# Kernel optimization log

Measured on AMD Instinct MI355X. Metric: run time of the kernel, lower is better.

Reference implementation:

```python
import jax, jax.numpy as jnp
import numpy as np

D_MODEL = 64  # angle_dist_dim
IN_CH = 256
EPS = 1e-6


def sinusoidal_embedding(e, d_model):
    # e: (N, K) -> (N, K, d_model), interleaved [sin0, cos0, sin1, cos1, ...]
    div_term = jnp.exp(jnp.arange(0, d_model, 2, dtype=jnp.float32) * (-np.log(10000.0) / d_model))
    om = e[..., None] * div_term  # (N, K, d_model//2)
    emb = jnp.stack([jnp.sin(om), jnp.cos(om)], axis=-1)  # (N, K, d/2, 2)
    return emb.reshape(e.shape + (d_model,))


def setup_inputs() -> dict:
    key = jax.random.key(0)
    ks = jax.random.split(key, 5)
    N, K, C = 40000, 16, IN_CH
    triplet_dim = 2 * C + D_MODEL  # 576
    x = jax.random.normal(ks[0], (N, C), dtype=jnp.float32)
    pos = jax.random.normal(ks[1], (N, 3), dtype=jnp.float32) * 10.0
    anchor_indices = jnp.arange(N, dtype=jnp.int32)
    corner_indices = jax.random.randint(ks[2], (N, K, 2), 0, N, dtype=jnp.int32)
    corner_masks = jnp.ones((N, K), dtype=bool)
    Wqkv_w = jax.random.normal(ks[3], (3 * C, triplet_dim), dtype=jnp.float32) / np.sqrt(triplet_dim)
    Wqkv_b = jax.random.normal(ks[4], (3 * C,), dtype=jnp.float32) * 0.01
    return {"x": x, "pos": pos, "anchor_indices": anchor_indices,
            "corner_indices": corner_indices, "corner_masks": corner_masks,
            "Wqkv_w": Wqkv_w, "Wqkv_b": Wqkv_b}


def reference(x, pos, anchor_indices, corner_indices, corner_masks, Wqkv_w, Wqkv_b):
    N, C = x.shape
    padded_x = jnp.concatenate([x, jnp.zeros((1, C), x.dtype)], axis=0)
    padded_pos = jnp.concatenate([pos, jnp.zeros((1, 3), pos.dtype)], axis=0)

    anchor_p = padded_pos[anchor_indices]            # (Na, 3)
    v0 = padded_pos[corner_indices[:, :, 0]] - anchor_p[:, None]  # (Na, K, 3)
    v1 = padded_pos[corner_indices[:, :, 1]] - anchor_p[:, None]
    v0 = jax.lax.stop_gradient(v0).at[:, :, 2].set(0.0)  # zero z (detached geometry)
    v1 = jax.lax.stop_gradient(v1).at[:, :, 2].set(0.0)

    cos_values = jnp.sum(v0 * v1, axis=-1) / (
        jnp.linalg.norm(v0, axis=-1) * jnp.linalg.norm(v1, axis=-1) + EPS)
    # z-component of cross product (x,y only since z was zeroed)
    sin_z = v0[..., 0] * v1[..., 1] - v0[..., 1] * v1[..., 0]
    reorder = sin_z < 0  # (Na, K)

    ci = jnp.where(reorder[..., None], corner_indices[:, :, ::-1], corner_indices)

    nv0 = jax.lax.stop_gradient(padded_pos[ci[:, :, 0]] - anchor_p[:, None]).at[:, :, 2].set(0.0)
    nv1 = jax.lax.stop_gradient(padded_pos[ci[:, :, 1]] - anchor_p[:, None]).at[:, :, 2].set(0.0)
    new_sin_z = nv0[..., 0] * nv1[..., 1] - nv0[..., 1] * nv1[..., 0]
    # corner_masks is all-True so boolean selection == full flatten (static shape)
    triplet_false_masks = ((new_sin_z < -1e-6) & corner_masks).reshape(-1)

    angle_features = jax.lax.stop_gradient(sinusoidal_embedding(cos_values, D_MODEL))
    triplet_feats = jnp.concatenate(
        [padded_x[ci[:, :, 0]], padded_x[ci[:, :, 1]], angle_features], axis=-1)  # (Na, K, 576)

    qkv = triplet_feats @ Wqkv_w.T + Wqkv_b            # (Na, K, 3C)
    qkv = qkv.reshape(qkv.shape[0], qkv.shape[1], 3, C)
    q, k, v = qkv[:, :, 0], qkv[:, :, 1], qkv[:, :, 2]

    scores = jnp.einsum('nqc,nkc->nqk', q, k) / np.sqrt(C)
    attn = jax.nn.softmax(scores, axis=-1)
    attn_feats = jnp.einsum('nqk,nkc->nqc', attn, v)   # (Na, K, C)

    mask_f = corner_masks.astype(attn_feats.dtype)
    denom = jnp.sum(mask_f, axis=1, keepdims=True)     # (Na, 1)
    mean_feats = jnp.sum(attn_feats * mask_f[..., None], axis=1) / denom  # (Na, C)

    x_messages = jnp.zeros_like(x).at[anchor_indices].set(mean_feats)
    out = jnp.concatenate([x, x_messages], axis=1)     # (N, 2C), triplet_mlp_method='concat'
    return out, triplet_false_masks
```

## Files before the change

### kernel.cpp

```cpp
#include <hip/hip_runtime.h>

typedef unsigned short u16;
typedef __attribute__((ext_vector_type(8))) short short8v;
typedef __attribute__((ext_vector_type(4))) float float4v;

__device__ __forceinline__ float bf2f(u16 u) {
  union { unsigned int i; float f; } v; v.i = ((unsigned int)u) << 16; return v.f;
}
__device__ __forceinline__ u16 f2bf(float f) {
  union { unsigned int i; float f; } v; v.f = f;
  unsigned int r = v.i + 0x7fffu + ((v.i >> 16) & 1u);
  return (u16)(r >> 16);
}
__device__ __forceinline__ float4v mfma_bf16(short8v a, short8v b, float4v c) {
  return __builtin_amdgcn_mfma_f32_16x16x32_bf16(a, b, c, 0, 0, 0);
}

__global__ __launch_bounds__(256) void prep_kernel(const float* __restrict__ W,
                                                   u16* __restrict__ Bt,
                                                   u16* __restrict__ W2t) {
  int j = blockIdx.x;
  int c = threadIdx.x;
  const float* wr = W + (size_t)j * 576;
  Bt[(size_t)j * 256 + c]         = f2bf(wr[c]);
  Bt[(size_t)(768 + j) * 256 + c] = f2bf(wr[256 + c]);
  if (c < 64) W2t[(size_t)j * 64 + c] = f2bf(wr[512 + c]);
}

__global__ __launch_bounds__(256) void gemm_kernel(const float* __restrict__ A,
                                                   const u16* __restrict__ Bt,
                                                   u16* __restrict__ Y, int M) {
  __shared__ __align__(16) u16 As[128][72];
  __shared__ __align__(16) u16 Bs[128][72];
  int tid = threadIdx.x;
  int row0 = blockIdx.x * 128, col0 = blockIdx.y * 128;
  int w = tid >> 6, l = tid & 63;
  int wr = w >> 1, wc = w & 1;
  int lr = l & 15, lq = l >> 4;

  float4v acc[4][4];
#pragma unroll
  for (int mi = 0; mi < 4; mi++)
#pragma unroll
    for (int ni = 0; ni < 4; ni++) acc[mi][ni] = (float4v)0.f;

  for (int k0 = 0; k0 < 256; k0 += 64) {
#pragma unroll
    for (int i = 0; i < 4; i++) {
      int chunk = tid + i * 256;
      int r = chunk >> 3;
      int kc = (chunk & 7) * 8;
      int gr = row0 + r;
      short8v av = (short8v)0;
      if (gr < M) {
        float4 f0 = *(const float4*)(A + (size_t)gr * 256 + k0 + kc);
        float4 f1 = *(const float4*)(A + (size_t)gr * 256 + k0 + kc + 4);
        av[0] = (short)f2bf(f0.x); av[1] = (short)f2bf(f0.y);
        av[2] = (short)f2bf(f0.z); av[3] = (short)f2bf(f0.w);
        av[4] = (short)f2bf(f1.x); av[5] = (short)f2bf(f1.y);
        av[6] = (short)f2bf(f1.z); av[7] = (short)f2bf(f1.w);
      }
      *(short8v*)&As[r][kc] = av;
      short8v bv = *(const short8v*)(Bt + (size_t)(col0 + r) * 256 + k0 + kc);
      *(short8v*)&Bs[r][kc] = bv;
    }
    __syncthreads();
#pragma unroll
    for (int s = 0; s < 2; s++) {
      int kb = s * 32 + lq * 8;
      short8v af[4], bf[4];
#pragma unroll
      for (int mi = 0; mi < 4; mi++)
        af[mi] = *(const short8v*)&As[wr * 64 + mi * 16 + lr][kb];
#pragma unroll
      for (int ni = 0; ni < 4; ni++)
        bf[ni] = *(const short8v*)&Bs[wc * 64 + ni * 16 + lr][kb];
#pragma unroll
      for (int mi = 0; mi < 4; mi++)
#pragma unroll
        for (int ni = 0; ni < 4; ni++)
          acc[mi][ni] = mfma_bf16(af[mi], bf[ni], acc[mi][ni]);
    }
    __syncthreads();
  }
#pragma unroll
  for (int mi = 0; mi < 4; mi++)
#pragma unroll
    for (int ni = 0; ni < 4; ni++) {
      int rbase = row0 + wr * 64 + mi * 16 + lq * 4;
      int c = col0 + wc * 64 + ni * 16 + lr;
#pragma unroll
      for (int j = 0; j < 4; j++) {
        int r = rbase + j;
        if (r < M) Y[(size_t)r * 1536 + c] = f2bf(acc[mi][ni][j]);
      }
    }
}

__global__ __launch_bounds__(256) void triplet_kernel(
    const float* __restrict__ x, const float* __restrict__ pos,
    const int* __restrict__ anchor, const int* __restrict__ corner,
    const float* __restrict__ bias, const u16* __restrict__ Y,
    const u16* __restrict__ W2t, float* __restrict__ out, int N) {
  __shared__ float s_cos[16];
  __shared__ float s_div[32];
  __shared__ int s_i0[16], s_i1[16];
  __shared__ __align__(16) u16 s_qkv[16][776];

  int n = blockIdx.x;
  if (n >= N) return;
  int tid = threadIdx.x;
  int w = tid >> 6;
  int l = tid & 63;
  int lr = l & 15, lq = l >> 4, kg = lq * 8;
  int a = anchor[n];

  if (tid < 32) s_div[tid] = __expf(-0.28782313662425572f * (float)tid);
  if (tid < 16) {
    int t = tid;
    int2 ci = ((const int2*)corner)[n * 16 + t];
    float ax = pos[(size_t)a * 3], ay = pos[(size_t)a * 3 + 1];
    float v0x = pos[(size_t)ci.x * 3]     - ax;
    float v0y = pos[(size_t)ci.x * 3 + 1] - ay;
    float v1x = pos[(size_t)ci.y * 3]     - ax;
    float v1y = pos[(size_t)ci.y * 3 + 1] - ay;
    float dot = v0x * v1x + v0y * v1y;
    float n0 = sqrtf(v0x * v0x + v0y * v0y);
    float n1 = sqrtf(v1x * v1x + v1y * v1y);
    s_cos[t] = dot / (n0 * n1 + 1e-6f);
    float sinz = v0x * v1y - v0y * v1x;
    bool sw = sinz < 0.f;
    s_i0[t] = sw ? ci.y : ci.x;
    s_i1[t] = sw ? ci.x : ci.y;
    __builtin_nontemporal_store(0.0f, &out[(size_t)N * 512 + (size_t)n * 16 + t]);
  }
  if (tid < 64) {
    const float4v* src = (const float4v*)(x + (size_t)n * 256);
    float4v* dst = (float4v*)(out + (size_t)n * 512);
    float4v v = __builtin_nontemporal_load(src + tid);
    __builtin_nontemporal_store(v, dst + tid);
  }
  __syncthreads();

  float cosv = s_cos[lr];
  short8v a0, a1;
#pragma unroll
  for (int jj = 0; jj < 4; jj++) {
    int kh = (kg >> 1) + jj;
    float om0 = cosv * s_div[kh];
    a0[2 * jj]     = (short)f2bf(__sinf(om0));
    a0[2 * jj + 1] = (short)f2bf(__cosf(om0));
    float om1 = cosv * s_div[16 + kh];
    a1[2 * jj]     = (short)f2bf(__sinf(om1));
    a1[2 * jj + 1] = (short)f2bf(__cosf(om1));
  }
  int i0r[4], i1r[4];
#pragma unroll
  for (int j = 0; j < 4; j++) {
    int t = lq * 4 + j;
    i0r[j] = s_i0[t];
    i1r[j] = s_i1[t];
  }

  for (int u = 0; u < 12; u++) {
    int nt = w * 12 + u;
    int col = nt * 16 + lr;
    short8v b0 = *(const short8v*)(W2t + (size_t)col * 64 + kg);
    short8v b1 = *(const short8v*)(W2t + (size_t)col * 64 + 32 + kg);
    float4v acc = (float4v)0.f;
    acc = mfma_bf16(a0, b0, acc);
    acc = mfma_bf16(a1, b1, acc);
    float bs = bias[col];
#pragma unroll
    for (int j = 0; j < 4; j++) {
      float v = acc[j] + bs + bf2f(Y[(size_t)i0r[j] * 1536 + col]) +
                bf2f(Y[(size_t)i1r[j] * 1536 + 768 + col]);
      s_qkv[lq * 4 + j][col] = f2bf(v);
    }
  }
  __syncthreads();

  float4v sa = (float4v)0.f;
#pragma unroll
  for (int cs = 0; cs < 8; cs++) {
    short8v qf = *(const short8v*)&s_qkv[lr][cs * 32 + kg];
    short8v kf = *(const short8v*)&s_qkv[lr][256 + cs * 32 + kg];
    sa = mfma_bf16(qf, kf, sa);
  }
  float wsum = 0.f;
#pragma unroll
  for (int j = 0; j < 4; j++) {
    float s = sa[j] * 0.0625f;
    float m = s;
    m = fmaxf(m, __shfl_xor(m, 1));
    m = fmaxf(m, __shfl_xor(m, 2));
    m = fmaxf(m, __shfl_xor(m, 4));
    m = fmaxf(m, __shfl_xor(m, 8));
    float e = __expf(s - m);
    float sm = e;
    sm += __shfl_xor(sm, 1);
    sm += __shfl_xor(sm, 2);
    sm += __shfl_xor(sm, 4);
    sm += __shfl_xor(sm, 8);
    wsum += e / sm;
  }
  wsum += __shfl_xor(wsum, 16);
  wsum += __shfl_xor(wsum, 32);
  wsum *= 0.0625f;

  int c = (w << 6) + l;
  float o = 0.f;
#pragma unroll
  for (int kk = 0; kk < 16; kk++) {
    float wk = __shfl(wsum, kk);
    o += wk * bf2f(s_qkv[kk][512 + c]);
  }
  __builtin_nontemporal_store(o, &out[(size_t)a * 512 + 256 + c]);
}

extern "C" void kernel_launch(void* const* d_in, const int* in_sizes, int n_in,
                              void* d_out, int out_size, void* d_ws, size_t ws_size,
                              hipStream_t stream) {
  const float* x    = (const float*)d_in[0];
  const float* pos  = (const float*)d_in[1];
  const int* anchor = (const int*)d_in[2];
  const int* corner = (const int*)d_in[3];
  const float* W    = (const float*)d_in[5];
  const float* bias = (const float*)d_in[6];
  float* out = (float*)d_out;
  int N = in_sizes[2];

  char* wsb = (char*)d_ws;
  u16* Bt  = (u16*)wsb;
  u16* W2t = (u16*)(wsb + 786432);
  u16* Y   = (u16*)(wsb + 786432 + 98304);

  prep_kernel<<<768, 256, 0, stream>>>(W, Bt, W2t);
  gemm_kernel<<<dim3((N + 127) / 128, 12), 256, 0, stream>>>(x, Bt, Y, N);
  triplet_kernel<<<N, 256, 0, stream>>>(x, pos, anchor, corner, bias, Y, W2t, out, N);
}
```

Measured before the change: 804.8 us.

## Reassociate V projection after attention averaging to shrink precomputed Y

Before, the kernel precomputed V for every node and gathered it per triplet. Now the attention-weighted mean is applied to the raw gathered x rows and the angle embeddings first, using linearity. The resulting 512-wide per-anchor features S are multiplied by the V weights in a second GEMM that adds bias and accumulates into the output. This drops a third of the first GEMM output and the V gathers, but adds fp32 x gathers in the triplet kernel, a new GEMM pass over N, and a read-modify-write of the output.

```diff
diff --git a/kernel.cpp b/kernel.cpp
--- a/kernel.cpp
+++ b/kernel.cpp
@@ -18,13 +18,21 @@
 
 __global__ __launch_bounds__(256) void prep_kernel(const float* __restrict__ W,
                                                    u16* __restrict__ Bt,
-                                                   u16* __restrict__ W2t) {
+                                                   u16* __restrict__ W2qk,
+                                                   u16* __restrict__ Wvt,
+                                                   u16* __restrict__ Wvat) {
   int j = blockIdx.x;
   int c = threadIdx.x;
   const float* wr = W + (size_t)j * 576;
   Bt[(size_t)j * 256 + c]         = f2bf(wr[c]);
-  Bt[(size_t)(768 + j) * 256 + c] = f2bf(wr[256 + c]);
-  if (c < 64) W2t[(size_t)j * 64 + c] = f2bf(wr[512 + c]);
+  Bt[(size_t)(512 + j) * 256 + c] = f2bf(wr[256 + c]);
+  if (c < 64) W2qk[(size_t)j * 64 + c] = f2bf(wr[512 + c]);
+  if (j < 256) {
+    const float* wv = W + (size_t)(512 + j) * 576;
+    Wvt[(size_t)j * 512 + c]       = f2bf(wv[c]);
+    Wvt[(size_t)j * 512 + 256 + c] = f2bf(wv[256 + c]);
+    if (c < 64) Wvat[(size_t)j * 64 + c] = f2bf(wv[512 + c]);
+  }
 }
 
 __global__ __launch_bounds__(256) void gemm_kernel(const float* __restrict__ A,
@@ -92,7 +100,7 @@
 #pragma unroll
       for (int j = 0; j < 4; j++) {
         int r = rbase + j;
-        if (r < M) Y[(size_t)r * 1536 + c] = f2bf(acc[mi][ni][j]);
+        if (r < M) Y[(size_t)r * 1024 + c] = f2bf(acc[mi][ni][j]);
       }
     }
 }
@@ -100,12 +108,14 @@
 __global__ __launch_bounds__(256) void triplet_kernel(
     const float* __restrict__ x, const float* __restrict__ pos,
     const int* __restrict__ anchor, const int* __restrict__ corner,
-    const float* __restrict__ bias, const u16* __restrict__ Y,
-    const u16* __restrict__ W2t, float* __restrict__ out, int N) {
+    const float* __restrict__ bias, const u16* __restrict__ Yqk,
+    const u16* __restrict__ W2qk, const u16* __restrict__ Wvat,
+    u16* __restrict__ S, float* __restrict__ out, int N) {
   __shared__ float s_cos[16];
   __shared__ float s_div[32];
+  __shared__ float s_sang[64];
   __shared__ int s_i0[16], s_i1[16];
-  __shared__ __align__(16) u16 s_qkv[16][776];
+  __shared__ __align__(16) u16 s_qk[16][520];
 
   int n = blockIdx.x;
   if (n >= N) return;
@@ -162,20 +172,20 @@
     i1r[j] = s_i1[t];
   }
 
-  for (int u = 0; u < 12; u++) {
-    int nt = w * 12 + u;
+  for (int u = 0; u < 8; u++) {
+    int nt = w * 8 + u;
     int col = nt * 16 + lr;
-    short8v b0 = *(const short8v*)(W2t + (size_t)col * 64 + kg);
-    short8v b1 = *(const short8v*)(W2t + (size_t)col * 64 + 32 + kg);
+    short8v b0 = *(const short8v*)(W2qk + (size_t)col * 64 + kg);
+    short8v b1 = *(const short8v*)(W2qk + (size_t)col * 64 + 32 + kg);
     float4v acc = (float4v)0.f;
     acc = mfma_bf16(a0, b0, acc);
     acc = mfma_bf16(a1, b1, acc);
     float bs = bias[col];
 #pragma unroll
     for (int j = 0; j < 4; j++) {
-      float v = acc[j] + bs + bf2f(Y[(size_t)i0r[j] * 1536 + col]) +
-                bf2f(Y[(size_t)i1r[j] * 1536 + 768 + col]);
-      s_qkv[lq * 4 + j][col] = f2bf(v);
+      float v = acc[j] + bs + bf2f(Yqk[(size_t)i0r[j] * 1024 + col]) +
+                bf2f(Yqk[(size_t)i1r[j] * 1024 + 512 + col]);
+      s_qk[lq * 4 + j][col] = f2bf(v);
     }
   }
   __syncthreads();
@@ -183,8 +193,8 @@
   float4v sa = (float4v)0.f;
 #pragma unroll
   for (int cs = 0; cs < 8; cs++) {
-    short8v qf = *(const short8v*)&s_qkv[lr][cs * 32 + kg];
-    short8v kf = *(const short8v*)&s_qkv[lr][256 + cs * 32 + kg];
+    short8v qf = *(const short8v*)&s_qk[lr][cs * 32 + kg];
+    short8v kf = *(const short8v*)&s_qk[lr][256 + cs * 32 + kg];
     sa = mfma_bf16(qf, kf, sa);
   }
   float wsum = 0.f;
@@ -208,14 +218,114 @@
   wsum += __shfl_xor(wsum, 32);
   wsum *= 0.0625f;
 
-  int c = (w << 6) + l;
-  float o = 0.f;
-#pragma unroll
-  for (int kk = 0; kk < 16; kk++) {
-    float wk = __shfl(wsum, kk);
-    o += wk * bf2f(s_qkv[kk][512 + c]);
-  }
-  __builtin_nontemporal_store(o, &out[(size_t)a * 512 + 256 + c]);
+  {
+    int c = tid;
+    float acc0 = 0.f, acc1 = 0.f;
+#pragma unroll
+    for (int t = 0; t < 16; t++) {
+      float wt = __shfl(wsum, t);
+      int r0 = s_i0[t], r1 = s_i1[t];
+      acc0 += wt * x[(size_t)r0 * 256 + c];
+      acc1 += wt * x[(size_t)r1 * 256 + c];
+    }
+    S[(size_t)n * 512 + c]       = f2bf(acc0);
+    S[(size_t)n * 512 + 256 + c] = f2bf(acc1);
+  }
+
+  if (tid < 64) {
+    float dv = s_div[tid >> 1];
+    float sj = 0.f;
+#pragma unroll
+    for (int t = 0; t < 16; t++) {
+      float wt = __shfl(wsum, t);
+      float om = s_cos[t] * dv;
+      sj += wt * ((tid & 1) ? __cosf(om) : __sinf(om));
+    }
+    s_sang[tid] = sj;
+  }
+  __syncthreads();
+  {
+    int c = tid;
+    float ov = 0.f;
+    const u16* wvr = Wvat + (size_t)c * 64;
+#pragma unroll
+    for (int jj = 0; jj < 8; jj++) {
+      short8v wv8 = *(const short8v*)(wvr + jj * 8);
+#pragma unroll
+      for (int m = 0; m < 8; m++) ov += bf2f((u16)wv8[m]) * s_sang[jj * 8 + m];
+    }
+    out[(size_t)a * 512 + 256 + c] = ov;
+  }
+}
+
+__global__ __launch_bounds__(256) void gemm2_kernel(const u16* __restrict__ S,
+                                                    const u16* __restrict__ Wvt,
+                                                    const float* __restrict__ bias,
+                                                    const int* __restrict__ anchor,
+                                                    float* __restrict__ out, int M) {
+  __shared__ __align__(16) u16 As[128][72];
+  __shared__ __align__(16) u16 Bs[128][72];
+  int tid = threadIdx.x;
+  int row0 = blockIdx.x * 128, col0 = blockIdx.y * 128;
+  int w = tid >> 6, l = tid & 63;
+  int wr = w >> 1, wc = w & 1;
+  int lr = l & 15, lq = l >> 4;
+
+  float4v acc[4][4];
+#pragma unroll
+  for (int mi = 0; mi < 4; mi++)
+#pragma unroll
+    for (int ni = 0; ni < 4; ni++) acc[mi][ni] = (float4v)0.f;
+
+  for (int k0 = 0; k0 < 512; k0 += 64) {
+#pragma unroll
+    for (int i = 0; i < 4; i++) {
+      int chunk = tid + i * 256;
+      int r = chunk >> 3;
+      int kc = (chunk & 7) * 8;
+      int gr = row0 + r;
+      short8v av = (short8v)0;
+      if (gr < M) av = *(const short8v*)(S + (size_t)gr * 512 + k0 + kc);
+      *(short8v*)&As[r][kc] = av;
+      short8v bv = *(const short8v*)(Wvt + (size_t)(col0 + r) * 512 + k0 + kc);
+      *(short8v*)&Bs[r][kc] = bv;
+    }
+    __syncthreads();
+#pragma unroll
+    for (int s = 0; s < 2; s++) {
+      int kb = s * 32 + lq * 8;
+      short8v af[4], bf[4];
+#pragma unroll
+      for (int mi = 0; mi < 4; mi++)
+        af[mi] = *(const short8v*)&As[wr * 64 + mi * 16 + lr][kb];
+#pragma unroll
+      for (int ni = 0; ni < 4; ni++)
+        bf[ni] = *(const short8v*)&Bs[wc * 64 + ni * 16 + lr][kb];
+#pragma unroll
+      for (int mi = 0; mi < 4; mi++)
+#pragma unroll
+        for (int ni = 0; ni < 4; ni++)
+          acc[mi][ni] = mfma_bf16(af[mi], bf[ni], acc[mi][ni]);
+    }
+    __syncthreads();
+  }
+#pragma unroll
+  for (int mi = 0; mi < 4; mi++)
+#pragma unroll
+    for (int ni = 0; ni < 4; ni++) {
+      int rbase = row0 + wr * 64 + mi * 16 + lq * 4;
+      int c = col0 + wc * 64 + ni * 16 + lr;
+      float bv = bias[512 + c];
+#pragma unroll
+      for (int j = 0; j < 4; j++) {
+        int r = rbase + j;
+        if (r < M) {
+          int a = anchor[r];
+          size_t o = (size_t)a * 512 + 256 + c;
+          out[o] = out[o] + acc[mi][ni][j] + bv;
+        }
+      }
+    }
 }
 
 extern "C" void kernel_launch(void* const* d_in, const int* in_sizes, int n_in,
@@ -231,11 +341,17 @@
   int N = in_sizes[2];
 
   char* wsb = (char*)d_ws;
-  u16* Bt  = (u16*)wsb;
-  u16* W2t = (u16*)(wsb + 786432);
-  u16* Y   = (u16*)(wsb + 786432 + 98304);
-
-  prep_kernel<<<768, 256, 0, stream>>>(W, Bt, W2t);
-  gemm_kernel<<<dim3((N + 127) / 128, 12), 256, 0, stream>>>(x, Bt, Y, N);
-  triplet_kernel<<<N, 256, 0, stream>>>(x, pos, anchor, corner, bias, Y, W2t, out, N);
-}
+  u16* Bt   = (u16*)wsb;
+  u16* W2qk = (u16*)(wsb + 524288);
+  u16* Wvt  = (u16*)(wsb + 589824);
+  u16* Wvat = (u16*)(wsb + 851968);
+  u16* Yqk  = (u16*)(wsb + 884736);
+  u16* S    = (u16*)(wsb + 884736 + 81920000);
+
+  prep_kernel<<<512, 256, 0, stream>>>(W, Bt, W2qk, Wvt, Wvat);
+  gemm_kernel<<<dim3((N + 127) / 128, 8), 256, 0, stream>>>(x, Bt, Yqk, N);
+  triplet_kernel<<<N, 256, 0, stream>>>(x, pos, anchor, corner, bias, Yqk,
+                                        W2qk, Wvat, S, out, N);
+  gemm2_kernel<<<dim3((N + 127) / 128, 2), 256, 0, stream>>>(S, Wvt, bias,
+                                                             anchor, out, N);
+}
```

Measured after the change: 887.5 us. 10.3% more time.
